# Optimization experiments

Measured on AMD Instinct MI355X. Metric: run time of the kernel, lower is better.

The kernel has to match this reference:

```python
import jax, jax.numpy as jnp
import numpy as np

NEG_SLOPE = 0.2  # PyG GATConv default negative_slope


def _entity_embedding(r_emb, attr_emb, femb_w, femb_b):
    # r_emb: [N, Dr], attr_emb: [N, A, Da]; femb: Linear(Da->De)
    rp = r_emb @ femb_w.T + femb_b                      # [N, De]
    ap = attr_emb @ femb_w.T + femb_b                   # [N, A, De]
    scores = jnp.einsum('nd,nad->na', rp, ap)           # [N, A]
    att = jax.nn.softmax(scores, axis=1)
    return jnp.einsum('na,nad->nd', att, ap)            # [N, De]


def _gat_conv(x, edge_index, w, a_src, a_dst, bias):
    # Single-head GATConv (PyG defaults: add_self_loops=True, negative_slope=0.2)
    n = x.shape[0]
    loop = jnp.arange(n, dtype=edge_index.dtype)
    src = jnp.concatenate([edge_index[0], loop])
    dst = jnp.concatenate([edge_index[1], loop])
    h = x @ w.T                                         # [N, Do]
    alpha_s = h @ a_src                                 # [N]
    alpha_d = h @ a_dst                                 # [N]
    e = jax.nn.leaky_relu(alpha_s[src] + alpha_d[dst], NEG_SLOPE)  # [E+N]
    m = jax.ops.segment_max(e, dst, num_segments=n)
    ex = jnp.exp(e - m[dst])
    denom = jax.ops.segment_sum(ex, dst, num_segments=n)
    alpha = ex / denom[dst]
    out = jax.ops.segment_sum(alpha[:, None] * h[src], dst, num_segments=n)
    return out + bias


def setup_inputs() -> dict:
    key = jax.random.key(0)
    ks = jax.random.split(key, 16)
    N, A, E = 50000, 16, 800000
    NUM_ATTR, NUM_REL = 50000, 500
    Da = De = Dr = 128
    Din1 = De + Dr  # gat1 input dim
    inp = {
        'h_attributes': jax.random.randint(ks[0], (N, A), 0, NUM_ATTR),
        't_attributes': jax.random.randint(ks[1], (N, A), 0, NUM_ATTR),
        'r_idx': jax.random.randint(ks[2], (N,), 0, NUM_REL),
        'edge_index': jax.random.randint(ks[3], (2, E), 0, N),
        'attr_table': jax.random.normal(ks[4], (NUM_ATTR, Da), jnp.float32),
        'rel_table': jax.random.normal(ks[5], (NUM_REL, Dr), jnp.float32),
        'femb_w': jax.random.normal(ks[6], (De, Da), jnp.float32) / np.sqrt(Da),
        'femb_b': jnp.zeros((De,), jnp.float32),
        'gat1_w': jax.random.normal(ks[7], (De, Din1), jnp.float32) / np.sqrt(Din1),
        'gat1_asrc': jax.random.normal(ks[8], (De,), jnp.float32) / np.sqrt(De),
        'gat1_adst': jax.random.normal(ks[9], (De,), jnp.float32) / np.sqrt(De),
        'gat1_b': jnp.zeros((De,), jnp.float32),
        'gat2_w': jax.random.normal(ks[10], (De, De), jnp.float32) / np.sqrt(De),
        'gat2_asrc': jax.random.normal(ks[11], (De,), jnp.float32) / np.sqrt(De),
        'gat2_adst': jax.random.normal(ks[12], (De,), jnp.float32) / np.sqrt(De),
        'gat2_b': jnp.zeros((De,), jnp.float32),
    }
    return inp


def reference(h_attributes, t_attributes, r_idx, edge_index,
              attr_table, rel_table, femb_w, femb_b,
              gat1_w, gat1_asrc, gat1_adst, gat1_b,
              gat2_w, gat2_asrc, gat2_adst, gat2_b):
    h_attr_emb = attr_table[h_attributes]               # [N, A, Da]
    t_attr_emb = attr_table[t_attributes]               # [N, A, Da]
    r_emb = rel_table[r_idx]                            # [N, Dr]
    h_emb = _entity_embedding(r_emb, h_attr_emb, femb_w, femb_b)  # [N, De]
    t_emb = _entity_embedding(r_emb, t_attr_emb, femb_w, femb_b)  # [N, De]
    # aggregate head/tail then concat relation -> [N, De + Dr] (matches gat1 in_dim)
    triple_emb = jnp.concatenate([h_emb + t_emb, r_emb], axis=1)
    x = _gat_conv(triple_emb, edge_index, gat1_w, gat1_asrc, gat1_adst, gat1_b)
    return _gat_conv(x, edge_index, gat2_w, gat2_asrc, gat2_adst, gat2_b)
```

## Files before the change

kernel.cpp:

```cpp
#include <hip/hip_runtime.h>
#include <math.h>

#define DE 128
#define NEG_SLOPE 0.2f
#define LOG2E 1.4426950408889634f
#define ESHIFT2 57.707801635559926f
#define ESHIFT_AGG 28.853900817779268f
#define EXP2(x) __builtin_amdgcn_exp2f(x)

typedef __attribute__((ext_vector_type(4))) float f4;
typedef __attribute__((ext_vector_type(2))) float f2;
typedef _Float16 half_t;
typedef __attribute__((ext_vector_type(2))) _Float16 h2;
typedef __attribute__((ext_vector_type(4))) _Float16 h4v;
typedef __attribute__((ext_vector_type(8))) _Float16 h8;

__device__ __forceinline__ float wave_red_bcast(float x) {
    union fi { float f; int i; };
    fi a; a.f = x;
    fi t;
    t.i = __builtin_amdgcn_update_dpp(0, a.i, 0x111, 0xf, 0xf, true); a.f += t.f;
    t.i = __builtin_amdgcn_update_dpp(0, a.i, 0x112, 0xf, 0xf, true); a.f += t.f;
    t.i = __builtin_amdgcn_update_dpp(0, a.i, 0x114, 0xf, 0xf, true); a.f += t.f;
    t.i = __builtin_amdgcn_update_dpp(0, a.i, 0x118, 0xf, 0xf, true); a.f += t.f;
    t.i = __builtin_amdgcn_update_dpp(0, a.i, 0x142, 0xa, 0xf, true); a.f += t.f;
    t.i = __builtin_amdgcn_update_dpp(0, a.i, 0x143, 0xc, 0xf, true); a.f += t.f;
    fi r; r.i = __builtin_amdgcn_readlane(a.i, 63);
    return r.f;
}

__device__ __forceinline__ float row16_allred(float x) {
    union fi { float f; int i; };
    fi a; a.f = x;
    fi t;
    t.i = __builtin_amdgcn_update_dpp(0, a.i, 0x121, 0xf, 0xf, true); a.f += t.f;
    t.i = __builtin_amdgcn_update_dpp(0, a.i, 0x122, 0xf, 0xf, true); a.f += t.f;
    t.i = __builtin_amdgcn_update_dpp(0, a.i, 0x124, 0xf, 0xf, true); a.f += t.f;
    t.i = __builtin_amdgcn_update_dpp(0, a.i, 0x128, 0xf, 0xf, true); a.f += t.f;
    return a.f;
}

__device__ __forceinline__ void count_body(int bid, const int* __restrict__ ei, int E, int N,
                                           int* __restrict__ cnt) {
    int e = bid * 256 + threadIdx.x;
    int total = E + N;
    if (e >= total) return;
    int dst = (e < E) ? ei[E + e] : (e - E);
    atomicAdd(&cnt[dst], 1);
}

__device__ void scan_body(const int* __restrict__ cnt, int n, int* __restrict__ indptr,
                          char* smem) {
    int* wsum = (int*)smem;
    int* btot = (int*)smem + 4;
    const int tid = threadIdx.x, lane = tid & 63, w = tid >> 6;
    int carry = 0;
    for (int base = 0; base < n; base += 1024) {
        int i0 = base + tid * 4;
        int4 v = {0, 0, 0, 0};
        if (i0 + 3 < n) v = *(const int4*)(cnt + i0);
        else {
            if (i0 < n)     v.x = cnt[i0];
            if (i0 + 1 < n) v.y = cnt[i0 + 1];
            if (i0 + 2 < n) v.z = cnt[i0 + 2];
        }
        int s = v.x + v.y + v.z + v.w;
        int x = s;
#pragma unroll
        for (int off = 1; off < 64; off <<= 1) {
            int t = __shfl_up(x, off, 64);
            if (lane >= off) x += t;
        }
        if (lane == 63) wsum[w] = x;
        __syncthreads();
        if (tid == 0) {
            int acc = 0;
#pragma unroll
            for (int k = 0; k < 4; ++k) { int t = wsum[k]; wsum[k] = acc; acc += t; }
            *btot = acc;
        }
        __syncthreads();
        int excl = carry + wsum[w] + (x - s);
        if (i0 < n)     indptr[i0]     = excl;
        if (i0 + 1 < n) indptr[i0 + 1] = excl + v.x;
        if (i0 + 2 < n) indptr[i0 + 2] = excl + v.x + v.y;
        if (i0 + 3 < n) indptr[i0 + 3] = excl + v.x + v.y + v.z;
        carry += *btot;
        __syncthreads();
    }
    if (tid == 0) indptr[n] = carry;
}

__device__ __forceinline__ void fill_body(int bid, const int* __restrict__ ei, int E, int N,
                                          const int* __restrict__ indptr,
                                          int* __restrict__ cur, int* __restrict__ adj) {
    int e = bid * 256 + threadIdx.x;
    int total = E + N;
    if (e >= total) return;
    int src, dst;
    if (e < E) { src = ei[e]; dst = ei[E + e]; }
    else       { src = dst = e - E; }
    int pos = indptr[dst] + atomicAdd(&cur[dst], 1);
    adj[pos] = src;
}

__device__ void rel_body(int bx, int sel, const float* __restrict__ in, int rows,
                         const float* __restrict__ W1, const float* __restrict__ bias1,
                         float* __restrict__ out1, const float* __restrict__ W2,
                         float* __restrict__ out2, char* smem) {
    const float* W; int ldw, wcol0; const float* bias; float* out;
    if (sel == 0) { W = W1; ldw = DE;     wcol0 = 0;  bias = bias1;   out = out1; }
    else          { W = W2; ldw = 2 * DE; wcol0 = DE; bias = nullptr; out = out2; }

    float* Wt = (float*)smem;
    const int tid = threadIdx.x;
#pragma unroll
    for (int it = 0; it < 16; ++it) {
        int idx = it * 256 + tid;
        int c = idx & 127, k4 = idx >> 7;
        f4 wv = *(const f4*)(W + (size_t)c * ldw + wcol0 + k4 * 4);
#pragma unroll
        for (int j = 0; j < 4; ++j) Wt[(4 * k4 + j) * 128 + c] = wv[j];
    }
    __syncthreads();

    const int RPT = 2;
    const int cgrp = tid & 15, rgrp = tid >> 4;
    const int c0 = cgrp * 4;
    const int row0 = bx * (16 * RPT) + rgrp * RPT;

    const float* rowp[RPT];
#pragma unroll
    for (int i = 0; i < RPT; ++i)
        rowp[i] = in + (size_t)min(row0 + i, rows - 1) * 128;

    float acc[RPT][8];
#pragma unroll
    for (int i = 0; i < RPT; ++i)
#pragma unroll
        for (int j = 0; j < 8; ++j) acc[i][j] = 0.f;

#pragma unroll 1
    for (int k = 0; k < 128; k += 4) {
        f4 a[RPT];
#pragma unroll
        for (int i = 0; i < RPT; ++i) a[i] = *(const f4*)(rowp[i] + k);
#pragma unroll
        for (int kk = 0; kk < 4; ++kk) {
            f4 b0 = *(const f4*)&Wt[(k + kk) * 128 + c0];
            f4 b1 = *(const f4*)&Wt[(k + kk) * 128 + c0 + 64];
#pragma unroll
            for (int i = 0; i < RPT; ++i) {
                float av = a[i][kk];
#pragma unroll
                for (int j = 0; j < 4; ++j) {
                    acc[i][j]     = fmaf(av, b0[j], acc[i][j]);
                    acc[i][j + 4] = fmaf(av, b1[j], acc[i][j + 4]);
                }
            }
        }
    }
    f4 bi0 = {0.f,0.f,0.f,0.f}, bi1 = {0.f,0.f,0.f,0.f};
    if (bias) { bi0 = *(const f4*)(bias + c0); bi1 = *(const f4*)(bias + c0 + 64); }
#pragma unroll
    for (int i = 0; i < RPT; ++i) {
        int r = row0 + i;
        if (r < rows) {
            f4 v0, v1;
#pragma unroll
            for (int j = 0; j < 4; ++j) { v0[j] = acc[i][j] + bi0[j]; v1[j] = acc[i][j+4] + bi1[j]; }
            *(f4*)(out + (size_t)r * 128 + c0) = v0;
            *(f4*)(out + (size_t)r * 128 + c0 + 64) = v1;
        }
    }
}

template <typename AT>
__device__ void gemm_mfma_body(int bid, const AT* __restrict__ A, int rows,
                               const float* __restrict__ W, int ldw, int wcol0,
                               const float* __restrict__ bias,
                               const float* __restrict__ addtab,
                               const int* __restrict__ addidx,
                               const float* __restrict__ avs,
                               const float* __restrict__ avd,
                               float* __restrict__ als,
                               float* __restrict__ ald,
                               half_t* __restrict__ out16, char* smem) {
    half_t* Wl = (half_t*)smem;
    float*  Dl = (float*)smem;

    const int tid = threadIdx.x;
    const int row0 = bid * 64;

    for (int i = tid * 4; i < 128 * 128; i += 1024) {
        int c = i >> 7, k = i & 127;
        f4 wv = *(const f4*)(W + (size_t)c * ldw + wcol0 + k);
        h4v hv = {(half_t)wv[0], (half_t)wv[1], (half_t)wv[2], (half_t)wv[3]};
        *(h4v*)(Wl + c * 136 + k) = hv;
    }
    __syncthreads();

    const int wv_id = tid >> 6, l = tid & 63, lr = l & 15, lk = l >> 4;
    const int r_a = min(row0 + wv_id * 16 + lr, rows - 1);

    h8 af[4];
#pragma unroll
    for (int ks = 0; ks < 4; ++ks) {
        if constexpr (sizeof(AT) == 4) {
            f4 a0 = *(const f4*)(A + (size_t)r_a * 128 + ks * 32 + lk * 8);
            f4 a1 = *(const f4*)(A + (size_t)r_a * 128 + ks * 32 + lk * 8 + 4);
            h8 v = {(half_t)a0[0], (half_t)a0[1], (half_t)a0[2], (half_t)a0[3],
                    (half_t)a1[0], (half_t)a1[1], (half_t)a1[2], (half_t)a1[3]};
            af[ks] = v;
        } else {
            af[ks] = *(const h8*)(A + (size_t)r_a * 128 + ks * 32 + lk * 8);
        }
    }

    f4 acc[8];
#pragma unroll
    for (int t = 0; t < 8; ++t) acc[t] = (f4){0.f, 0.f, 0.f, 0.f};
#pragma unroll
    for (int ks = 0; ks < 4; ++ks) {
#pragma unroll
        for (int t = 0; t < 8; ++t) {
            h8 bf = *(const h8*)(Wl + (t * 16 + lr) * 136 + ks * 32 + lk * 8);
            acc[t] = __builtin_amdgcn_mfma_f32_16x16x32_f16(af[ks], bf, acc[t], 0, 0, 0);
        }
    }
    __syncthreads();

#pragma unroll
    for (int t = 0; t < 8; ++t)
#pragma unroll
        for (int q = 0; q < 4; ++q)
            Dl[(wv_id * 16 + lk * 4 + q) * 132 + t * 16 + lr] = acc[t][q];
    __syncthreads();

    const int cl = (tid & 15) * 8;
    f4 bi0 = {0.f,0.f,0.f,0.f}, bi1 = bi0;
    if (bias) { bi0 = *(const f4*)(bias + cl); bi1 = *(const f4*)(bias + cl + 4); }
    f4 as0 = {0.f,0.f,0.f,0.f}, as1 = as0, ad0 = as0, ad1 = as0;
    if (als) {
        as0 = *(const f4*)(avs + cl) * LOG2E; as1 = *(const f4*)(avs + cl + 4) * LOG2E;
        ad0 = *(const f4*)(avd + cl) * LOG2E; ad1 = *(const f4*)(avd + cl + 4) * LOG2E;
    }
#pragma unroll
    for (int pass = 0; pass < 4; ++pass) {
        int lrow = pass * 16 + (tid >> 4);
        int r = row0 + lrow;
        bool ok = r < rows;
        f4 v0 = *(const f4*)(Dl + lrow * 132 + cl);
        f4 v1 = *(const f4*)(Dl + lrow * 132 + cl + 4);
        v0 += bi0; v1 += bi1;
        if (addtab) {
            int ri = addidx[min(r, rows - 1)];
            v0 += *(const f4*)(addtab + (size_t)ri * 128 + cl);
            v1 += *(const f4*)(addtab + (size_t)ri * 128 + cl + 4);
        }
        if (als) {
            float ps = 0.f, pd = 0.f;
#pragma unroll
            for (int j = 0; j < 4; ++j) {
                ps += v0[j] * as0[j] + v1[j] * as1[j];
                pd += v0[j] * ad0[j] + v1[j] * ad1[j];
            }
            ps = row16_allred(ps);
            pd = row16_allred(pd);
            if ((tid & 15) == 0 && ok) { als[r] = ps; ald[r] = pd; }
        }
        if (ok) {
            h8 o = {(half_t)v0[0], (half_t)v0[1], (half_t)v0[2], (half_t)v0[3],
                    (half_t)v1[0], (half_t)v1[1], (half_t)v1[2], (half_t)v1[3]};
            *(h8*)(out16 + (size_t)r * 128 + cl) = o;
        }
    }
}

__device__ void entity_body(int bid, const int* __restrict__ hA,
                            const int* __restrict__ tA,
                            const int* __restrict__ ridx,
                            const half_t* __restrict__ pattr,
                            const float* __restrict__ prel,
                            half_t* __restrict__ s_emb16, int N) {
    int w = (bid * 256 + (int)threadIdx.x) >> 6;
    if (w >= N) return;
    w = __builtin_amdgcn_readfirstlane(w);
    const int lane = threadIdx.x & 63;
    const int c = lane * 2;
    const int ri = ridx[w];
    const f2 rp = *(const f2*)(prel + (size_t)ri * 128 + c);
    const h2 rph = {(half_t)(rp[0] * LOG2E), (half_t)(rp[1] * LOG2E)};
    const float init = (lane == 0) ? -ESHIFT2 : 0.f;
    const int* __restrict__ hp = hA + (size_t)w * 16;
    const int* __restrict__ tp = tA + (size_t)w * 16;
    const char* __restrict__ pb = (const char*)pattr;
    const unsigned cb = (unsigned)lane << 2;

    f2 oh = {0.f, 0.f}, ot = {0.f, 0.f};
    float sh = 0.f, st = 0.f;

    auto ld = [&](int idx) -> h2 {
        return *(const h2*)(pb + (((unsigned)idx << 8) + cb));
    };

    h2 bh[2][4], bt[2][4];
#pragma unroll
    for (int q = 0; q < 4; ++q) {
        bh[0][q] = ld(hp[q]);
        bt[0][q] = ld(tp[q]);
    }
#pragma unroll
    for (int b = 0; b < 4; ++b) {
        const int cur = b & 1, nxt = cur ^ 1;
        if (b < 3) {
#pragma unroll
            for (int q = 0; q < 4; ++q) {
                bh[nxt][q] = ld(hp[4 * (b + 1) + q]);
                bt[nxt][q] = ld(tp[4 * (b + 1) + q]);
            }
        }
        float pph[4], ppt[4];
#pragma unroll
        for (int q = 0; q < 4; ++q) {
            pph[q] = __builtin_amdgcn_fdot2(rph, bh[cur][q], init, false);
            ppt[q] = __builtin_amdgcn_fdot2(rph, bt[cur][q], init, false);
        }
        float Sh[4], St[4];
#pragma unroll
        for (int q = 0; q < 4; ++q) {
            Sh[q] = wave_red_bcast(pph[q]);
            St[q] = wave_red_bcast(ppt[q]);
        }
#pragma unroll
        for (int q = 0; q < 4; ++q) {
            float wh = EXP2(Sh[q]);
            float wt = EXP2(St[q]);
            sh += wh; st += wt;
            oh[0] = fmaf(wh, (float)bh[cur][q][0], oh[0]);
            oh[1] = fmaf(wh, (float)bh[cur][q][1], oh[1]);
            ot[0] = fmaf(wt, (float)bt[cur][q][0], ot[0]);
            ot[1] = fmaf(wt, (float)bt[cur][q][1], ot[1]);
        }
    }
    float invh = 1.f / sh, invt = 1.f / st;
    h2 hv = {(half_t)(oh[0] * invh + ot[0] * invt),
             (half_t)(oh[1] * invh + ot[1] * invt)};
    *(h2*)(s_emb16 + (size_t)w * 128 + c) = hv;
}

__global__ __launch_bounds__(256) void k_count_attr(const int* __restrict__ ei, int E, int N,
                                                    int* __restrict__ cnt, int CB,
                                                    const float* __restrict__ attr, int NA,
                                                    const float* __restrict__ W,
                                                    const float* __restrict__ bias,
                                                    half_t* __restrict__ out16) {
    __shared__ alignas(16) char smem[128 * 136 * 2];
    int b = blockIdx.x;
    if (b < CB) count_body(b, ei, E, N, cnt);
    else gemm_mfma_body<float>(b - CB, attr, NA, W, DE, 0, bias, nullptr, nullptr,
                               nullptr, nullptr, nullptr, nullptr, out16, smem);
}

__global__ __launch_bounds__(256) void k_rel_scan(const float* __restrict__ in, int rows,
                                                  const float* __restrict__ W1,
                                                  const float* __restrict__ b1,
                                                  float* __restrict__ out1,
                                                  const float* __restrict__ W2,
                                                  float* __restrict__ out2, int RB,
                                                  const int* __restrict__ cnt, int n,
                                                  int* __restrict__ indptr) {
    __shared__ alignas(16) char smem[128 * 128 * 4];
    int b = blockIdx.x;
    if (b < 2 * RB) rel_body(b % RB, b / RB, in, rows, W1, b1, out1, W2, out2, smem);
    else scan_body(cnt, n, indptr, smem);
}

__global__ __launch_bounds__(256) void k_fill_entity(const int* __restrict__ ei, int E,
                                                     const int* __restrict__ indptr,
                                                     int* __restrict__ cur,
                                                     int* __restrict__ adj, int FB,
                                                     const int* __restrict__ hA,
                                                     const int* __restrict__ tA,
                                                     const int* __restrict__ ridx,
                                                     const half_t* __restrict__ pattr,
                                                     const float* __restrict__ prel,
                                                     half_t* __restrict__ s_emb16, int N) {
    int b = blockIdx.x;
    if (b < FB) fill_body(b, ei, E, N, indptr, cur, adj);
    else entity_body(b - FB, hA, tA, ridx, pattr, prel, s_emb16, N);
}

__global__ __launch_bounds__(256) void k_gemm_mfma_h(const half_t* __restrict__ A, int rows,
                                                     const float* __restrict__ W, int ldw, int wcol0,
                                                     const float* __restrict__ bias,
                                                     const float* __restrict__ addtab,
                                                     const int* __restrict__ addidx,
                                                     const float* __restrict__ avs,
                                                     const float* __restrict__ avd,
                                                     float* __restrict__ als,
                                                     float* __restrict__ ald,
                                                     half_t* __restrict__ out16) {
    __shared__ alignas(16) char smem[128 * 136 * 2];
    gemm_mfma_body<half_t>(blockIdx.x, A, rows, W, ldw, wcol0, bias, addtab, addidx,
                           avs, avd, als, ald, out16, smem);
}

__global__ __launch_bounds__(256) void k_aggregate(const int* __restrict__ indptr,
                                                   const int* __restrict__ adj,
                                                   const half_t* __restrict__ hsrc,
                                                   const float* __restrict__ als,
                                                   const float* __restrict__ ald,
                                                   const float* __restrict__ bias,
                                                   float* __restrict__ out,
                                                   half_t* __restrict__ out16, int N) {
    const int tid = threadIdx.x;
    const int wv = (blockIdx.x * 256 + tid) >> 6;
    const int nodeA = wv * 2;
    if (nodeA >= N) return;
    const int lane = tid & 63;
    const int node = min(nodeA + (lane >> 5), N - 1);
    const int sl = lane & 31;
    const int c = sl * 4;

    const int beg = indptr[node];
    const int deg = indptr[node + 1] - beg;
    const float adn = ald[node];
    const char* __restrict__ hb = (const char*)hsrc;
    const unsigned cb = (unsigned)sl << 3;

    float acc[4] = {0.f, 0.f, 0.f, 0.f};
    float exsum = 0.f;

    int cur[8], nxt[8];
#pragma unroll
    for (int q = 0; q < 8; ++q) cur[q] = adj[beg + q];

#pragma unroll 1
    for (int j0 = 0; j0 < deg; j0 += 8) {
        if (j0 + 8 < deg) {
#pragma unroll
            for (int q = 0; q < 8; ++q) nxt[q] = adj[beg + j0 + 8 + q];
        }
        int ss[8];
        float alv[8];
        h4v hv[8];
#pragma unroll
        for (int q = 0; q < 8; ++q)
            ss[q] = ((unsigned)cur[q] < (unsigned)N) ? cur[q] : 0;
#pragma unroll
        for (int q = 0; q < 8; ++q) alv[q] = als[ss[q]];
#pragma unroll
        for (int q = 0; q < 8; ++q)
            hv[q] = *(const h4v*)(hb + (((unsigned)ss[q] << 8) + cb));
#pragma unroll
        for (int q = 0; q < 8; ++q) {
            bool ok = (j0 + q) < deg;
            float e = alv[q] + adn;
            e = fmaxf(e, NEG_SLOPE * e);
            float ex = ok ? EXP2(e - ESHIFT_AGG) : 0.f;
            exsum += ex;
#pragma unroll
            for (int j = 0; j < 4; ++j) acc[j] = fmaf(ex, (float)hv[q][j], acc[j]);
        }
#pragma unroll
        for (int q = 0; q < 8; ++q) cur[q] = nxt[q];
    }

    float inv = 1.f / exsum;
    if (out) {
        f4 o;
#pragma unroll
        for (int j = 0; j < 4; ++j) o[j] = fmaf(acc[j], inv, bias[c + j]);
        *(f4*)(out + (size_t)node * 128 + c) = o;
    } else {
        h4v o;
#pragma unroll
        for (int j = 0; j < 4; ++j) o[j] = (half_t)fmaf(acc[j], inv, bias[c + j]);
        *(h4v*)(out16 + (size_t)node * 128 + c) = o;
    }
}

extern "C" void kernel_launch(void* const* d_in, const int* in_sizes, int n_in,
                              void* d_out, int out_size, void* d_ws, size_t ws_size,
                              hipStream_t stream) {
    const int*   hA   = (const int*)d_in[0];
    const int*   tA   = (const int*)d_in[1];
    const int*   rix  = (const int*)d_in[2];
    const int*   ei   = (const int*)d_in[3];
    const float* attr_table = (const float*)d_in[4];
    const float* rel_table  = (const float*)d_in[5];
    const float* femb_w = (const float*)d_in[6];
    const float* femb_b = (const float*)d_in[7];
    const float* g1w  = (const float*)d_in[8];
    const float* g1as = (const float*)d_in[9];
    const float* g1ad = (const float*)d_in[10];
    const float* g1b  = (const float*)d_in[11];
    const float* g2w  = (const float*)d_in[12];
    const float* g2as = (const float*)d_in[13];
    const float* g2ad = (const float*)d_in[14];
    const float* g2b  = (const float*)d_in[15];

    const int N  = in_sizes[2];
    const int E  = in_sizes[3] / 2;
    const int NA = in_sizes[4] / DE;
    const int NR = in_sizes[5] / DE;
    const int EN = E + N;

    char* p = (char*)d_ws;
    auto alloc = [&](size_t bytes) -> char* {
        char* q = p;
        p += (bytes + 255) & ~(size_t)255;
        return q;
    };
    half_t* proj16 = (half_t*)alloc((size_t)NA * DE * 2);
    half_t* s16    = (half_t*)alloc((size_t)N * DE * 2);
    half_t* h16    = (half_t*)alloc((size_t)N * DE * 2);
    half_t* x116   = (half_t*)alloc((size_t)N * DE * 2);
    float* prel    = (float*)alloc((size_t)NR * DE * 4);
    float* rel2    = (float*)alloc((size_t)NR * DE * 4);
    float* alps    = (float*)alloc((size_t)N * 4);
    float* alpd    = (float*)alloc((size_t)N * 4);
    int*   indptr  = (int*)alloc((size_t)(N + 1) * 4);
    int*   cnt     = (int*)alloc((size_t)N * 4);
    int*   cur     = (int*)alloc((size_t)N * 4);
    int*   adj     = (int*)alloc((size_t)(EN + 16) * 4);

    dim3 b256(256);
    const int CB = (EN + 255) / 256;
    const int MB = (NA + 63) / 64;
    const int RB = (NR + 31) / 32;
    const int FB = CB;
    const int EB = (N + 3) / 4;

    hipMemsetAsync(cnt, 0, (size_t)((char*)cur - (char*)cnt) + (size_t)N * 4, stream);

    k_count_attr<<<dim3(CB + MB), b256, 0, stream>>>(ei, E, N, cnt, CB,
                                                     attr_table, NA, femb_w, femb_b, proj16);

    k_rel_scan<<<dim3(2 * RB + 1), b256, 0, stream>>>(rel_table, NR, femb_w, femb_b, prel,
                                                      g1w, rel2, RB, cnt, N, indptr);

    k_fill_entity<<<dim3(FB + EB), b256, 0, stream>>>(ei, E, indptr, cur, adj, FB,
                                                      hA, tA, rix, proj16, prel, s16, N);

    k_gemm_mfma_h<<<dim3((N + 63) / 64), b256, 0, stream>>>(s16, N,
        g1w, 2 * DE, 0, nullptr, rel2, rix, g1as, g1ad, alps, alpd, h16);
    k_aggregate<<<dim3((N + 7) / 8), b256, 0, stream>>>(indptr, adj, h16, alps, alpd, g1b,
                                                        nullptr, x116, N);

    k_gemm_mfma_h<<<dim3((N + 63) / 64), b256, 0, stream>>>(x116, N,
        g2w, DE, 0, nullptr, nullptr, nullptr, g2as, g2ad, alps, alpd, h16);
    k_aggregate<<<dim3((N + 7) / 8), b256, 0, stream>>>(indptr, adj, h16, alps, alpd, g2b,
                                                        (float*)d_out, nullptr, N);
}
```

Before: 293.0 us.

## Regroup CSR fill with gemm1 and put GEMM blocks first in fused launches

The CSR adjacency fill moves out of the entity-embedding launch and into the first GAT projection GEMM launch, so the entity kernel runs alone and the fill overlaps with the GEMM. In both fused kernels the GEMM blocks now come first in block order and the lighter count/fill blocks second, so the long-running tiles are dispatched early. The total kernel count stays the same. The GEMM launch now needs 128x136x2 bytes of shared memory for the fill blocks too, which may lower occupancy for those blocks.

```diff
diff --git a/kernel.cpp b/kernel.cpp
--- a/kernel.cpp
+++ b/kernel.cpp
@@ -349,17 +349,17 @@
     *(h2*)(s_emb16 + (size_t)w * 128 + c) = hv;
 }
 
-__global__ __launch_bounds__(256) void k_count_attr(const int* __restrict__ ei, int E, int N,
-                                                    int* __restrict__ cnt, int CB,
-                                                    const float* __restrict__ attr, int NA,
+__global__ __launch_bounds__(256) void k_attr_count(const float* __restrict__ attr, int NA,
                                                     const float* __restrict__ W,
                                                     const float* __restrict__ bias,
-                                                    half_t* __restrict__ out16) {
+                                                    half_t* __restrict__ out16, int MB,
+                                                    const int* __restrict__ ei, int E, int N,
+                                                    int* __restrict__ cnt) {
     __shared__ alignas(16) char smem[128 * 136 * 2];
     int b = blockIdx.x;
-    if (b < CB) count_body(b, ei, E, N, cnt);
-    else gemm_mfma_body<float>(b - CB, attr, NA, W, DE, 0, bias, nullptr, nullptr,
-                               nullptr, nullptr, nullptr, nullptr, out16, smem);
+    if (b < MB) gemm_mfma_body<float>(b, attr, NA, W, DE, 0, bias, nullptr, nullptr,
+                                      nullptr, nullptr, nullptr, nullptr, out16, smem);
+    else count_body(b - MB, ei, E, N, cnt);
 }
 
 __global__ __launch_bounds__(256) void k_rel_scan(const float* __restrict__ in, int rows,
@@ -376,19 +376,33 @@
     else scan_body(cnt, n, indptr, smem);
 }
 
-__global__ __launch_bounds__(256) void k_fill_entity(const int* __restrict__ ei, int E,
-                                                     const int* __restrict__ indptr,
-                                                     int* __restrict__ cur,
-                                                     int* __restrict__ adj, int FB,
-                                                     const int* __restrict__ hA,
-                                                     const int* __restrict__ tA,
-                                                     const int* __restrict__ ridx,
-                                                     const half_t* __restrict__ pattr,
-                                                     const float* __restrict__ prel,
-                                                     half_t* __restrict__ s_emb16, int N) {
+__global__ __launch_bounds__(256) void k_entity(const int* __restrict__ hA,
+                                                const int* __restrict__ tA,
+                                                const int* __restrict__ ridx,
+                                                const half_t* __restrict__ pattr,
+                                                const float* __restrict__ prel,
+                                                half_t* __restrict__ s_emb16, int N) {
+    entity_body(blockIdx.x, hA, tA, ridx, pattr, prel, s_emb16, N);
+}
+
+__global__ __launch_bounds__(256) void k_gemm1_fill(const half_t* __restrict__ A, int rows,
+                                                    const float* __restrict__ W,
+                                                    const float* __restrict__ rel2,
+                                                    const int* __restrict__ rix,
+                                                    const float* __restrict__ avs,
+                                                    const float* __restrict__ avd,
+                                                    float* __restrict__ als,
+                                                    float* __restrict__ ald,
+                                                    half_t* __restrict__ out16, int GB,
+                                                    const int* __restrict__ ei, int E,
+                                                    const int* __restrict__ indptr,
+                                                    int* __restrict__ cur,
+                                                    int* __restrict__ adj) {
+    __shared__ alignas(16) char smem[128 * 136 * 2];
     int b = blockIdx.x;
-    if (b < FB) fill_body(b, ei, E, N, indptr, cur, adj);
-    else entity_body(b - FB, hA, tA, ridx, pattr, prel, s_emb16, N);
+    if (b < GB) gemm_mfma_body<half_t>(b, A, rows, W, 2 * DE, 0, nullptr, rel2, rix,
+                                       avs, avd, als, ald, out16, smem);
+    else fill_body(b - GB, ei, E, rows, indptr, cur, adj);
 }
 
 __global__ __launch_bounds__(256) void k_gemm_mfma_h(const half_t* __restrict__ A, int rows,
@@ -530,26 +544,27 @@
     const int CB = (EN + 255) / 256;
     const int MB = (NA + 63) / 64;
     const int RB = (NR + 31) / 32;
-    const int FB = CB;
+    const int GB = (N + 63) / 64;
     const int EB = (N + 3) / 4;
 
     hipMemsetAsync(cnt, 0, (size_t)((char*)cur - (char*)cnt) + (size_t)N * 4, stream);
 
-    k_count_attr<<<dim3(CB + MB), b256, 0, stream>>>(ei, E, N, cnt, CB,
-                                                     attr_table, NA, femb_w, femb_b, proj16);
+    k_attr_count<<<dim3(MB + CB), b256, 0, stream>>>(attr_table, NA, femb_w, femb_b,
+                                                     proj16, MB, ei, E, N, cnt);
 
     k_rel_scan<<<dim3(2 * RB + 1), b256, 0, stream>>>(rel_table, NR, femb_w, femb_b, prel,
                                                       g1w, rel2, RB, cnt, N, indptr);
 
-    k_fill_entity<<<dim3(FB + EB), b256, 0, stream>>>(ei, E, indptr, cur, adj, FB,
-                                                      hA, tA, rix, proj16, prel, s16, N);
-
-    k_gemm_mfma_h<<<dim3((N + 63) / 64), b256, 0, stream>>>(s16, N,
-        g1w, 2 * DE, 0, nullptr, rel2, rix, g1as, g1ad, alps, alpd, h16);
+    k_entity<<<dim3(EB), b256, 0, stream>>>(hA, tA, rix, proj16, prel, s16, N);
+
+    k_gemm1_fill<<<dim3(GB + CB), b256, 0, stream>>>(s16, N, g1w, rel2, rix,
+                                                     g1as, g1ad, alps, alpd, h16, GB,
+                                                     ei, E, indptr, cur, adj);
+
     k_aggregate<<<dim3((N + 7) / 8), b256, 0, stream>>>(indptr, adj, h16, alps, alpd, g1b,
                                                         nullptr, x116, N);
 
-    k_gemm_mfma_h<<<dim3((N + 63) / 64), b256, 0, stream>>>(x116, N,
+    k_gemm_mfma_h<<<dim3(GB), b256, 0, stream>>>(x116, N,
         g2w, DE, 0, nullptr, nullptr, nullptr, g2as, g2ad, alps, alpd, h16);
     k_aggregate<<<dim3((N + 7) / 8), b256, 0, stream>>>(indptr, adj, h16, alps, alpd, g2b,
                                                         (float*)d_out, nullptr, N);
```

Result: no change. 291.4 us (-0.5%).
